# Optimization experiments

Hardware: AMD Instinct MI355X
Metric: run time of the kernel (lower is better)

The kernel has to match this reference:

```python
import jax, jax.numpy as jnp
import numpy as np

B, T, F, M = 2, 600, 513, 5  # batch, frames, freq bins (FFT_SIZE=513), mics


def setup_inputs() -> dict:
    key = jax.random.key(0)
    k1, k2, k3 = jax.random.split(key, 3)
    spec_mix_t = jax.random.normal(k1, (B, T, F, M, 2), jnp.float32)
    corr_speech = jax.random.normal(k2, (B, T, F, M, M, 2), jnp.float32)
    corr_noise = jax.random.normal(k3, (B, T, F, M, M, 2), jnp.float32)
    return {"spec_mix_t": spec_mix_t, "corr_speech": corr_speech, "corr_noise": corr_noise}


def _as_complex(x):
    # torch.view_as_complex equivalent: last dim is (real, imag)
    return jax.lax.complex(x[..., 0], x[..., 1])


def reference(spec_mix_t, corr_speech, corr_noise):
    # [B,T,F,M,M] complex -> permute(0,2,1,3,4) -> [B,F,T,M,M]
    Phi_S = jnp.transpose(_as_complex(corr_speech), (0, 2, 1, 3, 4))
    Phi_N = jnp.transpose(_as_complex(corr_noise), (0, 2, 1, 3, 4))

    # diagonal loading: Phi_N += 1e-7 * (I + 1j*I)
    eye_c = (jnp.eye(M, dtype=jnp.float32) + 1j * jnp.eye(M, dtype=jnp.float32)).astype(Phi_N.dtype)
    Phi_N = Phi_N + 1e-7 * eye_c

    Phi_N_inv = jnp.linalg.inv(Phi_N)  # batched 5x5 complex inverse
    # complex_multi(Phi_N_inv, Phi_S) == complex matmul
    PNiPS = jnp.einsum('bftij,bftjk->bftik', Phi_N_inv, Phi_S)
    trace = jnp.einsum('bftii->bft', PNiPS)  # complex trace

    # a1 = PNiPS @ u1, u1 = e_1 -> first column
    a1 = PNiPS[..., :, 0]  # [B,F,T,M]

    eps = jnp.finfo(trace.real.dtype).eps
    W = a1 / (trace[..., None] + (eps + 1j * eps))  # MVDR weights [B,F,T,M]

    # mixture STFT: [B,T,F,M,2] -> complex [B,T,F,M] -> permute -> [B,F,T,M]
    stft_mix = jnp.transpose(_as_complex(spec_mix_t), (0, 2, 1, 3))

    # S_hat = W^H x  (per tf-bin inner product)
    S_hat = jnp.einsum('bftm,bftm->bft', jnp.conj(W), stft_mix)

    # est = stack([real, imag], -1) -> [B,F,T,2]
    return jnp.stack([S_hat.real, S_hat.imag], axis=-1)
```

## Files before the change

kernel.cpp:

```cpp
#include <hip/hip_runtime.h>


constexpr int MD = 5;
constexpr int TT = 600, FF = 513;
constexpr int TOTAL = 2 * TT * FF;
constexpr int CELLS = 64;
constexpr int NCH   = (TOTAL + CELLS - 1) / CELLS;
constexpr int MATB  = CELLS * 200;

typedef const __attribute__((address_space(1))) void* gas_t;
typedef __attribute__((address_space(3))) void* las_t;

__device__ __forceinline__ void load_lds16(const void* g, void* l) {
    __builtin_amdgcn_global_load_lds((gas_t)g, (las_t)l, 16, 0, 0);
}

#define WAITV(n) do { asm volatile("s_waitcnt vmcnt(" #n ")" ::: "memory"); \
                      __builtin_amdgcn_sched_barrier(0); } while (0)
#define WAITLGKM0 do { asm volatile("s_waitcnt lgkmcnt(0)" ::: "memory"); \
                       __builtin_amdgcn_sched_barrier(0); } while (0)
#define SCHED_FENCE() __builtin_amdgcn_sched_barrier(0)

__device__ __forceinline__ void cfma(float2& acc, float2 a, float2 b) {
    acc.x = __builtin_fmaf(a.x, b.x, acc.x);
    acc.y = __builtin_fmaf(a.x, b.y, acc.y);
    acc.x = __builtin_fmaf(-a.y, b.y, acc.x);
    acc.y = __builtin_fmaf(a.y, b.x, acc.y);
}
__device__ __forceinline__ void cfms(float2& acc, float2 a, float2 b) {
    acc.x = __builtin_fmaf(-a.x, b.x, acc.x);
    acc.y = __builtin_fmaf(-a.x, b.y, acc.y);
    acc.x = __builtin_fmaf(a.y, b.y, acc.x);
    acc.y = __builtin_fmaf(-a.y, b.x, acc.y);
}
__device__ __forceinline__ float2 cmul(float2 a, float2 b) {
    return make_float2(a.x * b.x - a.y * b.y, a.x * b.y + a.y * b.x);
}

__global__ __launch_bounds__(64) void mvdr_kernel(
    const float* __restrict__ spec,
    const float* __restrict__ corrS,
    const float* __restrict__ corrN,
    float* __restrict__ out)
{
    __shared__ __align__(16) unsigned char buf[MATB];
    const int tid    = threadIdx.x;
    const int c      = blockIdx.x;
    const int myCell = c * CELLS + tid;
    const bool full  = (c != NCH - 1);
    const size_t byteBase = (size_t)c * MATB;

    {
        const char* gN = (const char*)corrN + byteBase;
        if (full) {
#pragma unroll
            for (int i = 0; i < 13; ++i) {
                int off = i * 1024 + tid * 16;
                load_lds16(gN + off, (char*)buf + off);
            }
        } else {
            const int rem = TOTAL * 200 - (int)byteBase;
#pragma unroll
            for (int i = 0; i < 13; ++i) {
                int off = i * 1024 + tid * 16;
                if (off + 16 <= rem) load_lds16(gN + off, (char*)buf + off);
            }
        }
    }
    SCHED_FENCE();

    float2 xv[MD];
    {
        int cc = myCell < TOTAL ? myCell : TOTAL - 1;
        const float2* px = (const float2*)spec + (size_t)cc * MD;
#pragma unroll
        for (int m = 0; m < MD; ++m) xv[m] = px[m];
    }
    SCHED_FENCE();

    WAITV(5);
    float2 A[MD][MD];
    const float2* lm = (const float2*)(buf + tid * 200);
#pragma unroll
    for (int i = 0; i < MD; ++i)
#pragma unroll
        for (int j = 0; j < MD; ++j) A[i][j] = lm[i * MD + j];
    WAITLGKM0;

    {
        const char* gS = (const char*)corrS + byteBase;
        if (full) {
#pragma unroll
            for (int i = 0; i < 13; ++i) {
                int off = i * 1024 + tid * 16;
                load_lds16(gS + off, (char*)buf + off);
            }
        } else {
            const int rem = TOTAL * 200 - (int)byteBase;
#pragma unroll
            for (int i = 0; i < 13; ++i) {
                int off = i * 1024 + tid * 16;
                if (off + 16 <= rem) load_lds16(gS + off, (char*)buf + off);
            }
        }
    }
    SCHED_FENCE();

#pragma unroll
    for (int i = 0; i < MD; ++i) { A[i][i].x += 1e-7f; A[i][i].y += 1e-7f; }

#pragma unroll
    for (int k = 0; k < MD; ++k) {
        float2 p = A[k][k];
        float d  = 1.0f / (p.x * p.x + p.y * p.y);
        float2 ip = make_float2(p.x * d, -p.y * d);
        A[k][k] = ip;
#pragma unroll
        for (int cc = 0; cc < MD; ++cc) {
            if (cc == k) continue;
            A[k][cc] = cmul(A[k][cc], ip);
        }
#pragma unroll
        for (int i2 = 0; i2 < MD; ++i2) {
            if (i2 == k) continue;
            float2 fz = A[i2][k];
#pragma unroll
            for (int cc = 0; cc < MD; ++cc) {
                if (cc == k) continue;
                cfms(A[i2][cc], fz, A[k][cc]);
            }
            float2 tt = cmul(fz, ip);
            A[i2][k] = make_float2(-tt.x, -tt.y);
        }
    }

    WAITV(0);

    float2 tr0 = make_float2(0.f, 0.f), tr1 = make_float2(0.f, 0.f);
    float2 a1[MD] = {};
#pragma unroll
    for (int j = 0; j < MD; ++j) {
#pragma unroll
        for (int i = 0; i < MD; ++i) {
            float2 sv = lm[j * MD + i];
            if (((j + i) & 1) == 0) cfma(tr0, A[i][j], sv);
            else                    cfma(tr1, A[i][j], sv);
            if (i == 0) {
#pragma unroll
                for (int m = 0; m < MD; ++m) cfma(a1[m], A[m][j], sv);
            }
        }
    }
    const float eps = 1.1920929e-07f;
    float2 tr = make_float2(tr0.x + tr1.x + eps, tr0.y + tr1.y + eps);

    float2 z = make_float2(0.f, 0.f);
#pragma unroll
    for (int m = 0; m < MD; ++m) {
        z.x = __builtin_fmaf(a1[m].x, xv[m].x, z.x);
        z.y = __builtin_fmaf(a1[m].x, xv[m].y, z.y);
        z.x = __builtin_fmaf(a1[m].y, xv[m].y, z.x);
        z.y = __builtin_fmaf(-a1[m].y, xv[m].x, z.y);
    }

    float inv2 = 1.0f / (tr.x * tr.x + tr.y * tr.y);
    float shr = (z.x * tr.x - z.y * tr.y) * inv2;
    float shi = (z.x * tr.y + z.y * tr.x) * inv2;

    if (myCell < TOTAL) {
        int f  = myCell % FF;
        int bt = myCell / FF;
        int t  = bt % TT;
        int b  = bt / TT;
        float2* po = reinterpret_cast<float2*>(out);
        po[((size_t)b * FF + f) * TT + t] = make_float2(shr, shi);
    }
}

extern "C" void kernel_launch(void* const* d_in, const int* in_sizes, int n_in,
                              void* d_out, int out_size, void* d_ws, size_t ws_size,
                              hipStream_t stream) {
    const float* spec  = (const float*)d_in[0];
    const float* corrS = (const float*)d_in[1];
    const float* corrN = (const float*)d_in[2];
    float* out = (float*)d_out;

    mvdr_kernel<<<NCH, CELLS, 0, stream>>>(spec, corrS, corrN, out);
}
```

Before: 45.22 us.

## Convert to persistent grid-stride kernel with register prefetch of next noise tile

Launches a fixed grid of 3072 single-wave blocks that loop over 64-cell chunks instead of one block per chunk. Each iteration prefetches the next chunk's noise covariance into registers (float4 loads) while the current chunk is inverted, then writes it to LDS at the top of the next iteration. The speech covariance still streams via direct global-to-LDS loads. The goal is to overlap memory latency with the 5x5 inversion and cut block launch overhead. In exchange it uses many more VGPRs for prefetch buffers, relies on hand-counted vmcnt waits, and adds an odd volatile dummy load.

```diff
diff --git a/kernel.cpp b/kernel.cpp
--- a/kernel.cpp
+++ b/kernel.cpp
@@ -7,6 +7,8 @@
 constexpr int CELLS = 64;
 constexpr int NCH   = (TOTAL + CELLS - 1) / CELLS;
 constexpr int MATB  = CELLS * 200;
+constexpr int GRID  = 3072;
+constexpr long long CORRB = (long long)TOTAL * 200;
 
 typedef const __attribute__((address_space(1))) void* gas_t;
 typedef __attribute__((address_space(3))) void* las_t;
@@ -37,143 +39,156 @@
     return make_float2(a.x * b.x - a.y * b.y, a.x * b.y + a.y * b.x);
 }
 
-__global__ __launch_bounds__(64) void mvdr_kernel(
+__global__ __launch_bounds__(64, 3) void mvdr_kernel(
     const float* __restrict__ spec,
     const float* __restrict__ corrS,
     const float* __restrict__ corrN,
     float* __restrict__ out)
 {
     __shared__ __align__(16) unsigned char buf[MATB];
-    const int tid    = threadIdx.x;
-    const int c      = blockIdx.x;
-    const int myCell = c * CELLS + tid;
-    const bool full  = (c != NCH - 1);
-    const size_t byteBase = (size_t)c * MATB;
-
+    const int tid = threadIdx.x;
+    const char* gN = (const char*)corrN;
+    const char* gS = (const char*)corrS;
+
+    float4 nxt4[12];
+    float2 nxt2;
     {
-        const char* gN = (const char*)corrN + byteBase;
-        if (full) {
-#pragma unroll
-            for (int i = 0; i < 13; ++i) {
-                int off = i * 1024 + tid * 16;
-                load_lds16(gN + off, (char*)buf + off);
-            }
-        } else {
-            const int rem = TOTAL * 200 - (int)byteBase;
-#pragma unroll
-            for (int i = 0; i < 13; ++i) {
-                int off = i * 1024 + tid * 16;
-                if (off + 16 <= rem) load_lds16(gN + off, (char*)buf + off);
-            }
-        }
+        const long long nb = (long long)blockIdx.x * MATB;
+#pragma unroll
+        for (int i = 0; i < 12; ++i)
+            nxt4[i] = *reinterpret_cast<const float4*>(gN + nb + i * 1024 + tid * 16);
+        nxt2 = *reinterpret_cast<const float2*>(gN + nb + 12288 + tid * 8);
     }
     SCHED_FENCE();
-
-    float2 xv[MD];
     {
-        int cc = myCell < TOTAL ? myCell : TOTAL - 1;
-        const float2* px = (const float2*)spec + (size_t)cc * MD;
-#pragma unroll
-        for (int m = 0; m < MD; ++m) xv[m] = px[m];
+        float d = *(volatile const float*)gN;
+        asm volatile("" :: "v"(d));
     }
     SCHED_FENCE();
 
-    WAITV(5);
-    float2 A[MD][MD];
-    const float2* lm = (const float2*)(buf + tid * 200);
-#pragma unroll
-    for (int i = 0; i < MD; ++i)
-#pragma unroll
-        for (int j = 0; j < MD; ++j) A[i][j] = lm[i * MD + j];
-    WAITLGKM0;
-
-    {
-        const char* gS = (const char*)corrS + byteBase;
-        if (full) {
-#pragma unroll
-            for (int i = 0; i < 13; ++i) {
-                int off = i * 1024 + tid * 16;
-                load_lds16(gS + off, (char*)buf + off);
-            }
-        } else {
-            const int rem = TOTAL * 200 - (int)byteBase;
-#pragma unroll
-            for (int i = 0; i < 13; ++i) {
-                int off = i * 1024 + tid * 16;
-                if (off + 16 <= rem) load_lds16(gS + off, (char*)buf + off);
-            }
-        }
-    }
-    SCHED_FENCE();
-
-#pragma unroll
-    for (int i = 0; i < MD; ++i) { A[i][i].x += 1e-7f; A[i][i].y += 1e-7f; }
-
-#pragma unroll
-    for (int k = 0; k < MD; ++k) {
-        float2 p = A[k][k];
-        float d  = 1.0f / (p.x * p.x + p.y * p.y);
-        float2 ip = make_float2(p.x * d, -p.y * d);
-        A[k][k] = ip;
-#pragma unroll
-        for (int cc = 0; cc < MD; ++cc) {
-            if (cc == k) continue;
-            A[k][cc] = cmul(A[k][cc], ip);
-        }
-#pragma unroll
-        for (int i2 = 0; i2 < MD; ++i2) {
-            if (i2 == k) continue;
-            float2 fz = A[i2][k];
+    for (int c = blockIdx.x; c < NCH; c += GRID) {
+        WAITV(1);
+
+#pragma unroll
+        for (int i = 0; i < 12; ++i)
+            *reinterpret_cast<float4*>(buf + i * 1024 + tid * 16) = nxt4[i];
+        *reinterpret_cast<float2*>(buf + 12288 + tid * 8) = nxt2;
+
+        const float2* lm = reinterpret_cast<const float2*>(buf + tid * 200);
+        float2 A[MD][MD];
+#pragma unroll
+        for (int i = 0; i < MD; ++i)
+#pragma unroll
+            for (int j = 0; j < MD; ++j) A[i][j] = lm[i * MD + j];
+        WAITLGKM0;
+
+        const long long cb = (long long)c * MATB;
+        const long long remL = CORRB - cb;
+        const int remS = (int)(remL < (long long)MATB ? remL : (long long)MATB);
+
+#pragma unroll
+        for (int i = 0; i < 13; ++i) {
+            int off = i * 1024 + tid * 16;
+            if (off + 16 <= MATB) {
+                int goff = off <= remS - 16 ? off : remS - 16;
+                load_lds16(gS + cb + goff, buf + off);
+            }
+        }
+        SCHED_FENCE();
+
+        const int myCell = c * CELLS + tid;
+        float2 xv[MD];
+        {
+            int cc = myCell < TOTAL ? myCell : TOTAL - 1;
+            const float2* px = (const float2*)spec + (size_t)cc * MD;
+#pragma unroll
+            for (int m = 0; m < MD; ++m) xv[m] = px[m];
+        }
+        SCHED_FENCE();
+
+        const bool hasNext = (c + GRID) < NCH;
+        if (hasNext) {
+            const long long nb = (long long)(c + GRID) * MATB;
+#pragma unroll
+            for (int i = 0; i < 12; ++i) {
+                long long off = nb + i * 1024 + tid * 16;
+                if (off > CORRB - 16) off = CORRB - 16;
+                nxt4[i] = *reinterpret_cast<const float4*>(gN + off);
+            }
+            long long off2 = nb + 12288 + tid * 8;
+            if (off2 > CORRB - 8) off2 = CORRB - 8;
+            nxt2 = *reinterpret_cast<const float2*>(gN + off2);
+        }
+        SCHED_FENCE();
+
+#pragma unroll
+        for (int i = 0; i < MD; ++i) { A[i][i].x += 1e-7f; A[i][i].y += 1e-7f; }
+#pragma unroll
+        for (int k = 0; k < MD; ++k) {
+            float2 p = A[k][k];
+            float d  = 1.0f / (p.x * p.x + p.y * p.y);
+            float2 ip = make_float2(p.x * d, -p.y * d);
+            A[k][k] = ip;
 #pragma unroll
             for (int cc = 0; cc < MD; ++cc) {
                 if (cc == k) continue;
-                cfms(A[i2][cc], fz, A[k][cc]);
-            }
-            float2 tt = cmul(fz, ip);
-            A[i2][k] = make_float2(-tt.x, -tt.y);
-        }
-    }
-
-    WAITV(0);
-
-    float2 tr0 = make_float2(0.f, 0.f), tr1 = make_float2(0.f, 0.f);
-    float2 a1[MD] = {};
-#pragma unroll
-    for (int j = 0; j < MD; ++j) {
-#pragma unroll
-        for (int i = 0; i < MD; ++i) {
-            float2 sv = lm[j * MD + i];
-            if (((j + i) & 1) == 0) cfma(tr0, A[i][j], sv);
-            else                    cfma(tr1, A[i][j], sv);
-            if (i == 0) {
-#pragma unroll
-                for (int m = 0; m < MD; ++m) cfma(a1[m], A[m][j], sv);
-            }
-        }
-    }
-    const float eps = 1.1920929e-07f;
-    float2 tr = make_float2(tr0.x + tr1.x + eps, tr0.y + tr1.y + eps);
-
-    float2 z = make_float2(0.f, 0.f);
-#pragma unroll
-    for (int m = 0; m < MD; ++m) {
-        z.x = __builtin_fmaf(a1[m].x, xv[m].x, z.x);
-        z.y = __builtin_fmaf(a1[m].x, xv[m].y, z.y);
-        z.x = __builtin_fmaf(a1[m].y, xv[m].y, z.x);
-        z.y = __builtin_fmaf(-a1[m].y, xv[m].x, z.y);
-    }
-
-    float inv2 = 1.0f / (tr.x * tr.x + tr.y * tr.y);
-    float shr = (z.x * tr.x - z.y * tr.y) * inv2;
-    float shi = (z.x * tr.y + z.y * tr.x) * inv2;
-
-    if (myCell < TOTAL) {
-        int f  = myCell % FF;
-        int bt = myCell / FF;
-        int t  = bt % TT;
-        int b  = bt / TT;
-        float2* po = reinterpret_cast<float2*>(out);
-        po[((size_t)b * FF + f) * TT + t] = make_float2(shr, shi);
+                A[k][cc] = cmul(A[k][cc], ip);
+            }
+#pragma unroll
+            for (int i2 = 0; i2 < MD; ++i2) {
+                if (i2 == k) continue;
+                float2 fz = A[i2][k];
+#pragma unroll
+                for (int cc = 0; cc < MD; ++cc) {
+                    if (cc == k) continue;
+                    cfms(A[i2][cc], fz, A[k][cc]);
+                }
+                float2 tt = cmul(fz, ip);
+                A[i2][k] = make_float2(-tt.x, -tt.y);
+            }
+        }
+
+        if (hasNext) { WAITV(13); } else { WAITV(0); }
+
+        float2 tr0 = make_float2(0.f, 0.f), tr1 = make_float2(0.f, 0.f);
+        float2 a1[MD] = {};
+#pragma unroll
+        for (int j = 0; j < MD; ++j) {
+#pragma unroll
+            for (int i = 0; i < MD; ++i) {
+                float2 sv = lm[j * MD + i];
+                if (((j + i) & 1) == 0) cfma(tr0, A[i][j], sv);
+                else                    cfma(tr1, A[i][j], sv);
+                if (i == 0) {
+#pragma unroll
+                    for (int m = 0; m < MD; ++m) cfma(a1[m], A[m][j], sv);
+                }
+            }
+        }
+        const float eps = 1.1920929e-07f;
+        float2 tr = make_float2(tr0.x + tr1.x + eps, tr0.y + tr1.y + eps);
+
+        float2 z = make_float2(0.f, 0.f);
+#pragma unroll
+        for (int m = 0; m < MD; ++m) {
+            z.x = __builtin_fmaf(a1[m].x, xv[m].x, z.x);
+            z.y = __builtin_fmaf(a1[m].x, xv[m].y, z.y);
+            z.x = __builtin_fmaf(a1[m].y, xv[m].y, z.x);
+            z.y = __builtin_fmaf(-a1[m].y, xv[m].x, z.y);
+        }
+
+        float inv2 = 1.0f / (tr.x * tr.x + tr.y * tr.y);
+        float shr = (z.x * tr.x - z.y * tr.y) * inv2;
+        float shi = (z.x * tr.y + z.y * tr.x) * inv2;
+
+        if (myCell < TOTAL) {
+            int f  = myCell % FF;
+            int bt = myCell / FF;
+            int t  = bt % TT;
+            int b  = bt / TT;
+            float2* po = reinterpret_cast<float2*>(out);
+            po[((size_t)b * FF + f) * TT + t] = make_float2(shr, shi);
+        }
     }
 }
 
@@ -185,5 +200,5 @@
     const float* corrN = (const float*)d_in[2];
     float* out = (float*)d_out;
 
-    mvdr_kernel<<<NCH, CELLS, 0, stream>>>(spec, corrS, corrN, out);
-}
+    mvdr_kernel<<<GRID, CELLS, 0, stream>>>(spec, corrS, corrN, out);
+}
```

Measured after the change: 89.88 us. 1.99x slower.
